# Kernel tuning notes

Hardware: AMD Instinct MI355X
Metric: run time of the kernel (lower is better)

The kernel has to match this reference:

```python
import jax, jax.numpy as jnp
import numpy as np

N = 1024
C = 50000
D = 128
M_MARGIN = 0.35
S_SCALE = 30.0
LAMDA = 0.01


def setup_inputs() -> dict:
    key = jax.random.key(0)
    k1, k2, k3 = jax.random.split(key, 3)
    feature = jax.random.normal(k1, (N, D), dtype=jnp.float32)
    weight = jax.random.normal(k2, (C, D), dtype=jnp.float32)
    label = jax.random.randint(k3, (N,), 0, C, dtype=jnp.int64)
    return {"feature": feature, "weight": weight, "label": label}


def reference(feature, weight, label):
    eps = 1e-8  # torch CosineSimilarity eps
    f = feature / jnp.maximum(jnp.linalg.norm(feature, axis=-1, keepdims=True), eps)
    w = weight / jnp.maximum(jnp.linalg.norm(weight, axis=-1, keepdims=True), eps)
    cos = jnp.einsum("nd,cd->nc", f, w)  # [N, C] cosine similarities
    onehot = jax.nn.one_hot(label, C, dtype=cos.dtype)  # [N, C]
    # CosFace: subtract margin m from the target-class cosine, scale by s
    logits = S_SCALE * (cos - M_MARGIN * onehot)
    target_logit = S_SCALE * (jnp.take_along_axis(cos, label[:, None], axis=1)[:, 0] - M_MARGIN)
    # -log( exp(t) / (exp(t) + sum_{j != y} exp(s*cos_j)) ) = logsumexp(logits) - t
    lse = jax.nn.logsumexp(logits, axis=-1)  # [N]
    loss_lmc = jnp.mean(lse - target_logit)
    # center loss: 0.5 * sum_i ||f_i - w_{y_i}||^2
    diff = feature - weight[label]
    loss_c = 0.5 * jnp.sum(diff * diff)
    return loss_lmc + LAMDA * loss_c
```

## Files before the change

### kernel.cpp

```cpp
#include <hip/hip_runtime.h>

#define N_ROWS   1024
#define D_DIM    128
#define C_CLS    50000
#define C_PAD    50048
#define NCT64    782
#define NG       128
#define S_SCALE  30.0f
#define M_MARGIN 0.35f
#define EXP2_SCALE 43.2808512266689f

typedef short s8v __attribute__((ext_vector_type(8)));
typedef float f4v __attribute__((ext_vector_type(4)));

__device__ inline unsigned short f2bf(float f) {
    unsigned u = __float_as_uint(f);
    u += 0x7FFF + ((u >> 16) & 1);
    return (unsigned short)(u >> 16);
}
__device__ inline float bf2f(unsigned short h) {
    return __uint_as_float(((unsigned)h) << 16);
}
__device__ inline void load_lds16(const char* src, unsigned char* lds) {
    __builtin_amdgcn_global_load_lds(
        (const __attribute__((address_space(1))) void*)src,
        (__attribute__((address_space(3))) void*)lds, 16, 0, 0);
}

__global__ void norm_rows_fused(const float* __restrict__ weight,
                                const float* __restrict__ feature,
                                unsigned short* __restrict__ what,
                                unsigned short* __restrict__ fhat) {
    int wid = threadIdx.x >> 6, lane = threadIdx.x & 63;
    int r = blockIdx.x * 4 + wid;
    const float* src;
    unsigned short* dst;
    int srcRow, valid;
    if (r < C_PAD) {
        src = weight; dst = what; srcRow = r; valid = (r < C_CLS);
    } else {
        src = feature; dst = fhat; srcRow = r - C_PAD; valid = 1;
    }
    float2 v = make_float2(0.f, 0.f);
    if (valid) v = ((const float2*)src)[(size_t)srcRow * 64 + lane];
    float ss = v.x * v.x + v.y * v.y;
    #pragma unroll
    for (int s = 1; s < 64; s <<= 1) ss += __shfl_xor(ss, s, 64);
    float inv = valid ? 1.0f / fmaxf(sqrtf(ss), 1e-8f) : 0.f;
    ((ushort2*)dst)[(size_t)srcRow * 64 + lane] =
        make_ushort2(f2bf(v.x * inv), f2bf(v.y * inv));
}

__global__ __launch_bounds__(256, 4)
void gemm_exp_kernel(const short* __restrict__ fhat,
                     const short* __restrict__ what,
                     float* __restrict__ part2) {
    __shared__ __align__(16) unsigned char smem[32768];
    const int g   = blockIdx.x;
    const int rt  = blockIdx.y;
    const int tid = threadIdx.x;
    const int wid = tid >> 6;
    const int lane = tid & 63;
    const int nt = (g < 14) ? 7 : 6;

    const char* aSrc  = (const char*)fhat + (size_t)rt * 32768;
    const char* bBase = (const char*)what;

    #pragma unroll
    for (int i = 0; i < 8; i++) {
        int o = wid * 8192 + i * 1024 + lane * 16;
        int s = o ^ (((o >> 8) & 7) << 4);
        load_lds16(aSrc + s, smem + o);
    }
    __syncthreads();

    const int lrow = lane & 15;
    const int kgrp = lane >> 4;

    s8v afr[4][2];
    #pragma unroll
    for (int kk = 0; kk < 4; kk++)
        #pragma unroll
        for (int m = 0; m < 2; m++) {
            int row = wid * 32 + m * 16 + lrow;
            int b = (row * 256 + kk * 64 + kgrp * 16) ^ ((row & 7) << 4);
            afr[kk][m] = *(const s8v*)(smem + b);
        }
    __syncthreads();

    {
        const char* src = bBase + (size_t)g * 16384;
        #pragma unroll
        for (int i = 0; i < 4; i++) {
            int o = wid * 4096 + i * 1024 + lane * 16;
            int s = o ^ (((o >> 8) & 7) << 4);
            load_lds16(src + s, smem + o);
        }
    }
    __syncthreads();

    float esum[2][4];
    #pragma unroll
    for (int m = 0; m < 2; m++)
        #pragma unroll
        for (int j = 0; j < 4; j++) esum[m][j] = 0.f;

    int cur = 0;
    for (int t = 0; t < nt; ++t) {
        const int ct = g + 128 * t;
        if (t + 1 < nt) {
            const char* src = bBase + (size_t)(ct + 128) * 16384;
            unsigned char* dstb = smem + (cur ^ 1) * 16384;
            #pragma unroll
            for (int i = 0; i < 4; i++) {
                int o = wid * 4096 + i * 1024 + lane * 16;
                int s = o ^ (((o >> 8) & 7) << 4);
                load_lds16(src + s, dstb + o);
            }
        }

        const unsigned char* bb = smem + cur * 16384;
        f4v acc[2][4];
        f4v zero = {0.f, 0.f, 0.f, 0.f};
        #pragma unroll
        for (int m = 0; m < 2; m++)
            #pragma unroll
            for (int n = 0; n < 4; n++) acc[m][n] = zero;

        #pragma unroll
        for (int kk = 0; kk < 4; kk++) {
            s8v bfr[4];
            #pragma unroll
            for (int n = 0; n < 4; n++) {
                int row = n * 16 + lrow;
                int b = (row * 256 + kk * 64 + kgrp * 16) ^ ((row & 7) << 4);
                bfr[n] = *(const s8v*)(bb + b);
            }
            #pragma unroll
            for (int m = 0; m < 2; m++)
                #pragma unroll
                for (int n = 0; n < 4; n++)
                    acc[m][n] = __builtin_amdgcn_mfma_f32_16x16x32_bf16(
                        afr[kk][m], bfr[n], acc[m][n], 0, 0, 0);
        }

        if (ct != NCT64 - 1) {
            #pragma unroll
            for (int m = 0; m < 2; m++)
                #pragma unroll
                for (int n = 0; n < 4; n++)
                    #pragma unroll
                    for (int j = 0; j < 4; j++)
                        esum[m][j] += __builtin_amdgcn_exp2f(EXP2_SCALE * acc[m][n][j]);
        } else {
            int cbase = ct * 64;
            #pragma unroll
            for (int m = 0; m < 2; m++)
                #pragma unroll
                for (int n = 0; n < 4; n++) {
                    int gc = cbase + n * 16 + lrow;
                    #pragma unroll
                    for (int j = 0; j < 4; j++)
                        if (gc < C_CLS)
                            esum[m][j] += __builtin_amdgcn_exp2f(EXP2_SCALE * acc[m][n][j]);
                }
        }
        __syncthreads();
        cur ^= 1;
    }

    #pragma unroll
    for (int m = 0; m < 2; m++)
        #pragma unroll
        for (int j = 0; j < 4; j++) {
            float v = esum[m][j];
            v += __shfl_xor(v, 1, 64);
            v += __shfl_xor(v, 2, 64);
            v += __shfl_xor(v, 4, 64);
            v += __shfl_xor(v, 8, 64);
            if (lrow == 0) {
                int row = rt * 128 + wid * 32 + m * 16 + kgrp * 4 + j;
                part2[(size_t)row * NG + g] = v;
            }
        }
}

__global__ void finalize_rows_kernel(const float* __restrict__ part2,
                                     const unsigned short* __restrict__ fhat,
                                     const unsigned short* __restrict__ what,
                                     const float* __restrict__ feature,
                                     const float* __restrict__ weight,
                                     const int* __restrict__ label,
                                     float* __restrict__ rowval) {
    int wid = threadIdx.x >> 6, lane = threadIdx.x & 63;
    int n = blockIdx.x * 4 + wid;
    int y = label[n];

    float S = part2[(size_t)n * NG + lane] + part2[(size_t)n * NG + 64 + lane];

    float2 f2 = ((const float2*)feature)[(size_t)n * 64 + lane];
    float2 w2 = ((const float2*)weight)[(size_t)y * 64 + lane];
    float dx = f2.x - w2.x, dy = f2.y - w2.y;
    float cl = dx * dx + dy * dy;

    ushort2 fh = ((const ushort2*)fhat)[(size_t)n * 64 + lane];
    ushort2 wh = ((const ushort2*)what)[(size_t)y * 64 + lane];
    float cy = bf2f(fh.x) * bf2f(wh.x) + bf2f(fh.y) * bf2f(wh.y);

    #pragma unroll
    for (int s = 1; s < 64; s <<= 1) {
        S  += __shfl_xor(S, s, 64);
        cl += __shfl_xor(cl, s, 64);
        cy += __shfl_xor(cy, s, 64);
    }
    if (lane == 0) {
        float t  = S_SCALE * (cy - M_MARGIN);
        float Sp = S - __expf(S_SCALE * cy) + __expf(t);
        rowval[n] = (logf(Sp) - t) * (1.0f / (float)N_ROWS) + 0.005f * cl;
    }
}

__global__ void reduce_final_kernel(const float* __restrict__ rowval, float* __restrict__ out) {
    __shared__ float sbuf[4];
    int t = threadIdx.x;
    float v = rowval[t] + rowval[t + 256] + rowval[t + 512] + rowval[t + 768];
    #pragma unroll
    for (int s = 1; s < 64; s <<= 1) v += __shfl_xor(v, s, 64);
    if ((t & 63) == 0) sbuf[t >> 6] = v;
    __syncthreads();
    if (t == 0) out[0] = sbuf[0] + sbuf[1] + sbuf[2] + sbuf[3];
}

extern "C" void kernel_launch(void* const* d_in, const int* in_sizes, int n_in,
                              void* d_out, int out_size, void* d_ws, size_t ws_size,
                              hipStream_t stream) {
    const float* feature = (const float*)d_in[0];
    const float* weight  = (const float*)d_in[1];
    const int*   label   = (const int*)d_in[2];

    const size_t WS_NEEDED = 13602816;
    if (ws_size < WS_NEEDED) return;

    char* ws = (char*)d_ws;
    unsigned short* what = (unsigned short*)ws;
    unsigned short* fhat = (unsigned short*)(ws + 12812288);
    float*         part2 = (float*)(ws + 13074432);
    float*        rowval = (float*)(ws + 13598720);

    norm_rows_fused<<<dim3((C_PAD + N_ROWS) / 4), 256, 0, stream>>>(weight, feature, what, fhat);
    gemm_exp_kernel<<<dim3(NG, 8), 256, 0, stream>>>((const short*)fhat, (const short*)what, part2);
    finalize_rows_kernel<<<dim3(N_ROWS / 4), 256, 0, stream>>>(part2, fhat, what, feature, weight,
                                                               label, rowval);
    reduce_final_kernel<<<1, 256, 0, stream>>>(rowval, (float*)d_out);
}
```

Measured before the change: 37.81 us.

## Use 2x2 warp tiling with triple-buffered B loads and fewer column groups

The GEMM kernel now uses 96 column groups instead of 128. Each block's four warps form a 2x2 grid, so each warp holds 64 A rows and 32 B columns, which raises A-fragment reuse. The B tiles move to a three-stage LDS ring: prefetch runs two tiles ahead, and waits use explicit vmcnt counts plus raw barriers instead of __syncthreads. Partial sums double to 192 per row to cover the column split, and finalize and the workspace sizes are adjusted to match. The cost is 48KB of LDS per block, occupancy dropping to 3 blocks per CU, and 768 blocks in total. With the raw barriers it is unclear whether anything stops the ring slot being refilled while slower warps are still reading it.

```diff
diff --git a/kernel.cpp b/kernel.cpp
--- a/kernel.cpp
+++ b/kernel.cpp
@@ -5,7 +5,8 @@
 #define C_CLS    50000
 #define C_PAD    50048
 #define NCT64    782
-#define NG       128
+#define NG       96
+#define NPART    192
 #define S_SCALE  30.0f
 #define M_MARGIN 0.35f
 #define EXP2_SCALE 43.2808512266689f
@@ -51,17 +52,21 @@
         make_ushort2(f2bf(v.x * inv), f2bf(v.y * inv));
 }
 
-__global__ __launch_bounds__(256, 4)
+__global__ __launch_bounds__(256, 3)
 void gemm_exp_kernel(const short* __restrict__ fhat,
                      const short* __restrict__ what,
                      float* __restrict__ part2) {
-    __shared__ __align__(16) unsigned char smem[32768];
+    __shared__ __align__(16) unsigned char smem[49152];
     const int g   = blockIdx.x;
     const int rt  = blockIdx.y;
     const int tid = threadIdx.x;
     const int wid = tid >> 6;
     const int lane = tid & 63;
-    const int nt = (g < 14) ? 7 : 6;
+    const int lrow = lane & 15;
+    const int kgrp = lane >> 4;
+    const int wrow = wid >> 1;
+    const int wcol = wid & 1;
+    const int nt = (g < 14) ? 9 : 8;
 
     const char* aSrc  = (const char*)fhat + (size_t)rt * 32768;
     const char* bBase = (const char*)what;
@@ -74,43 +79,41 @@
     }
     __syncthreads();
 
-    const int lrow = lane & 15;
-    const int kgrp = lane >> 4;
-
-    s8v afr[4][2];
+    s8v afr[4][4];
     #pragma unroll
     for (int kk = 0; kk < 4; kk++)
         #pragma unroll
-        for (int m = 0; m < 2; m++) {
-            int row = wid * 32 + m * 16 + lrow;
+        for (int m = 0; m < 4; m++) {
+            int row = wrow * 64 + m * 16 + lrow;
             int b = (row * 256 + kk * 64 + kgrp * 16) ^ ((row & 7) << 4);
             afr[kk][m] = *(const s8v*)(smem + b);
         }
     __syncthreads();
 
-    {
-        const char* src = bBase + (size_t)g * 16384;
-        #pragma unroll
-        for (int i = 0; i < 4; i++) {
-            int o = wid * 4096 + i * 1024 + lane * 16;
-            int s = o ^ (((o >> 8) & 7) << 4);
-            load_lds16(src + s, smem + o);
-        }
-    }
-    __syncthreads();
-
-    float esum[2][4];
-    #pragma unroll
-    for (int m = 0; m < 2; m++)
+    #pragma unroll
+    for (int i = 0; i < 4; i++) {
+        int o = wid * 4096 + i * 1024 + lane * 16;
+        int s = o ^ (((o >> 8) & 7) << 4);
+        load_lds16(bBase + (size_t)g * 16384 + s, smem + o);
+        load_lds16(bBase + (size_t)(g + 96) * 16384 + s, smem + 16384 + o);
+    }
+
+    float esum[4][4];
+    #pragma unroll
+    for (int m = 0; m < 4; m++)
         #pragma unroll
         for (int j = 0; j < 4; j++) esum[m][j] = 0.f;
 
-    int cur = 0;
     for (int t = 0; t < nt; ++t) {
-        const int ct = g + 128 * t;
-        if (t + 1 < nt) {
-            const char* src = bBase + (size_t)(ct + 128) * 16384;
-            unsigned char* dstb = smem + (cur ^ 1) * 16384;
+        const int ct = g + 96 * t;
+        if (t + 1 < nt) asm volatile("s_waitcnt vmcnt(4)" ::: "memory");
+        else            asm volatile("s_waitcnt vmcnt(0)" ::: "memory");
+        __builtin_amdgcn_s_barrier();
+        __builtin_amdgcn_sched_barrier(0);
+
+        if (t + 2 < nt) {
+            const char* src = bBase + (size_t)(ct + 192) * 16384;
+            unsigned char* dstb = smem + ((t + 2) % 3) * 16384;
             #pragma unroll
             for (int i = 0; i < 4; i++) {
                 int o = wid * 4096 + i * 1024 + lane * 16;
@@ -119,58 +122,54 @@
             }
         }
 
-        const unsigned char* bb = smem + cur * 16384;
-        f4v acc[2][4];
+        const unsigned char* bb = smem + (t % 3) * 16384;
+        f4v acc[4][2];
         f4v zero = {0.f, 0.f, 0.f, 0.f};
         #pragma unroll
-        for (int m = 0; m < 2; m++)
-            #pragma unroll
-            for (int n = 0; n < 4; n++) acc[m][n] = zero;
+        for (int m = 0; m < 4; m++) { acc[m][0] = zero; acc[m][1] = zero; }
 
         #pragma unroll
         for (int kk = 0; kk < 4; kk++) {
-            s8v bfr[4];
-            #pragma unroll
-            for (int n = 0; n < 4; n++) {
-                int row = n * 16 + lrow;
+            s8v bfr[2];
+            #pragma unroll
+            for (int n = 0; n < 2; n++) {
+                int row = wcol * 32 + n * 16 + lrow;
                 int b = (row * 256 + kk * 64 + kgrp * 16) ^ ((row & 7) << 4);
                 bfr[n] = *(const s8v*)(bb + b);
             }
             #pragma unroll
-            for (int m = 0; m < 2; m++)
+            for (int m = 0; m < 4; m++) {
+                acc[m][0] = __builtin_amdgcn_mfma_f32_16x16x32_bf16(
+                    afr[kk][m], bfr[0], acc[m][0], 0, 0, 0);
+                acc[m][1] = __builtin_amdgcn_mfma_f32_16x16x32_bf16(
+                    afr[kk][m], bfr[1], acc[m][1], 0, 0, 0);
+            }
+        }
+
+        if (ct != NCT64 - 1) {
+            #pragma unroll
+            for (int m = 0; m < 4; m++)
                 #pragma unroll
-                for (int n = 0; n < 4; n++)
-                    acc[m][n] = __builtin_amdgcn_mfma_f32_16x16x32_bf16(
-                        afr[kk][m], bfr[n], acc[m][n], 0, 0, 0);
-        }
-
-        if (ct != NCT64 - 1) {
-            #pragma unroll
-            for (int m = 0; m < 2; m++)
-                #pragma unroll
-                for (int n = 0; n < 4; n++)
+                for (int n = 0; n < 2; n++)
                     #pragma unroll
                     for (int j = 0; j < 4; j++)
                         esum[m][j] += __builtin_amdgcn_exp2f(EXP2_SCALE * acc[m][n][j]);
         } else {
-            int cbase = ct * 64;
-            #pragma unroll
-            for (int m = 0; m < 2; m++)
+            #pragma unroll
+            for (int n = 0; n < 2; n++) {
+                int gc = ct * 64 + wcol * 32 + n * 16 + lrow;
                 #pragma unroll
-                for (int n = 0; n < 4; n++) {
-                    int gc = cbase + n * 16 + lrow;
+                for (int m = 0; m < 4; m++)
                     #pragma unroll
                     for (int j = 0; j < 4; j++)
                         if (gc < C_CLS)
                             esum[m][j] += __builtin_amdgcn_exp2f(EXP2_SCALE * acc[m][n][j]);
-                }
-        }
-        __syncthreads();
-        cur ^= 1;
-    }
-
-    #pragma unroll
-    for (int m = 0; m < 2; m++)
+            }
+        }
+    }
+
+    #pragma unroll
+    for (int m = 0; m < 4; m++)
         #pragma unroll
         for (int j = 0; j < 4; j++) {
             float v = esum[m][j];
@@ -179,8 +178,8 @@
             v += __shfl_xor(v, 4, 64);
             v += __shfl_xor(v, 8, 64);
             if (lrow == 0) {
-                int row = rt * 128 + wid * 32 + m * 16 + kgrp * 4 + j;
-                part2[(size_t)row * NG + g] = v;
+                int row = rt * 128 + wrow * 64 + m * 16 + kgrp * 4 + j;
+                part2[(size_t)row * NPART + g * 2 + wcol] = v;
             }
         }
 }
@@ -196,7 +195,8 @@
     int n = blockIdx.x * 4 + wid;
     int y = label[n];
 
-    float S = part2[(size_t)n * NG + lane] + part2[(size_t)n * NG + 64 + lane];
+    const float* p = part2 + (size_t)n * NPART;
+    float S = p[lane] + p[64 + lane] + p[128 + lane];
 
     float2 f2 = ((const float2*)feature)[(size_t)n * 64 + lane];
     float2 w2 = ((const float2*)weight)[(size_t)y * 64 + lane];
@@ -238,14 +238,14 @@
     const float* weight  = (const float*)d_in[1];
     const int*   label   = (const int*)d_in[2];
 
-    const size_t WS_NEEDED = 13602816;
+    const size_t WS_NEEDED = 13864960;
     if (ws_size < WS_NEEDED) return;
 
     char* ws = (char*)d_ws;
     unsigned short* what = (unsigned short*)ws;
     unsigned short* fhat = (unsigned short*)(ws + 12812288);
     float*         part2 = (float*)(ws + 13074432);
-    float*        rowval = (float*)(ws + 13598720);
+    float*        rowval = (float*)(ws + 13860864);
 
     norm_rows_fused<<<dim3((C_PAD + N_ROWS) / 4), 256, 0, stream>>>(weight, feature, what, fhat);
     gemm_exp_kernel<<<dim3(NG, 8), 256, 0, stream>>>((const short*)fhat, (const short*)what, part2);
```

Result: no change. 38.53 us (+1.9%).
